# Kernel optimization log

Hardware: AMD Instinct MI355X
Metric: run time of the kernel (lower is better)

The kernel has to match this reference:

```python
import jax, jax.numpy as jnp
import numpy as np

B, P, N, H = 8, 12, 5000, 8
E = 50000
NB = 8
TD0, TD1 = 16, 64
MAX_STEPS = 500


def _proj(x, w1, b1, w2, b2):
    # Projection: Linear -> ReLU -> Linear
    return jax.nn.relu(x @ w1 + b1) @ w2 + b2


def _ln(x, w, b, eps=1e-5):
    # LayerNorm over last two dims [N, H] with affine params [N, H]
    m = jnp.mean(x, axis=(-2, -1), keepdims=True)
    v = jnp.mean((x - m) ** 2, axis=(-2, -1), keepdims=True)
    return (x - m) * jax.lax.rsqrt(v + eps) * w + b


def _time_table():
    # DiffTimeEmbedding buffer: [MAX_STEPS, 2*TD0]
    steps = jnp.arange(MAX_STEPS, dtype=jnp.float32)[:, None]
    dims = jnp.arange(TD0, dtype=jnp.float32)[None, :]
    e = steps * 10.0 ** (dims * 4.0 / TD0)
    return jnp.concatenate([jnp.sin(e), jnp.cos(e)], axis=1)


def setup_inputs() -> dict:
    key = jax.random.key(0)
    ks = jax.random.split(key, 40)
    rn = lambda k, s, sc=0.1: jax.random.normal(k, s, jnp.float32) * sc
    return {
        'x': jax.random.normal(ks[0], (B, P, N), jnp.float32),
        'cond': jax.random.normal(ks[1], (B, P, N, H), jnp.float32),
        'pos': jax.random.normal(ks[2], (N, H), jnp.float32),
        'time': jax.random.randint(ks[3], (B,), 0, MAX_STEPS),
        'edge_index': jax.random.randint(ks[4], (2, E), 0, N),
        'te_w1': rn(ks[5], (2 * TD0, TD1)), 'te_b1': rn(ks[6], (TD1,)),
        'te_w2': rn(ks[7], (TD1, TD1)), 'te_b2': rn(ks[8], (TD1,)),
        'in_w1': rn(ks[9], (1, H)), 'in_b1': rn(ks[10], (H,)),
        'in_w2': rn(ks[11], (H, H)), 'in_b2': rn(ks[12], (H,)),
        'pos_w1': rn(ks[13], (H, H)), 'pos_b1': rn(ks[14], (H,)),
        'pos_w2': rn(ks[15], (H, H)), 'pos_b2': rn(ks[16], (H,)),
        'attn': jax.random.normal(ks[17], (NB + 1, 1), jnp.float32),
        'bt_w1': rn(ks[18], (NB, TD1, H)), 'bt_b1': rn(ks[19], (NB, H)),
        'bt_w2': rn(ks[20], (NB, H, H)), 'bt_b2': rn(ks[21], (NB, H)),
        'bc_w1': rn(ks[22], (NB, H, H)), 'bc_b1': rn(ks[23], (NB, H)),
        'bc_w2': rn(ks[24], (NB, H, H)), 'bc_b2': rn(ks[25], (NB, H)),
        'gn_w': 1.0 + rn(ks[26], (NB, N, H), 0.05), 'gn_b': rn(ks[27], (NB, N, H), 0.05),
        'tn_w': 1.0 + rn(ks[28], (NB, N, H), 0.05), 'tn_b': rn(ks[29], (NB, N, H), 0.05),
        'cv_w': rn(ks[30], (NB, P, P)), 'cv_b': rn(ks[31], (NB, P)),
        'out_w1': rn(ks[32], (H, H)), 'out_b1': rn(ks[33], (H,)),
        'out_w2': rn(ks[34], (H, 1)), 'out_b2': rn(ks[35], (1,)),
    }


def _forward(x, cond, pos, te_w1, te_b1, te_w2, te_b2, in_w1, in_b1, in_w2, in_b2,
             pos_w1, pos_b1, pos_w2, pos_b2, attn, bt_w1, bt_b1, bt_w2, bt_b2,
             bc_w1, bc_b1, bc_w2, bc_b2, gn_w, gn_b, tn_w, tn_b, cv_w, cv_b,
             out_w1, out_b1, out_w2, out_b2, time, edge_index):
    # diffusion-time embedding -> [B, TD1]
    te = _time_table()[time]
    te = jax.nn.silu(te @ te_w1 + te_b1)
    te = jax.nn.silu(te @ te_w2 + te_b2)
    # input + positional projection -> [B, P, N, H]
    h = _proj(x[..., None], in_w1, in_b1, in_w2, in_b2)
    h = h + _proj(pos, pos_w1, pos_b1, pos_w2, pos_b2)
    # LGConv symmetric GCN norm (no self loops), shared across blocks
    src, dst = edge_index[0], edge_index[1]
    deg = jnp.zeros((N,), h.dtype).at[dst].add(1.0)
    dinv = jnp.where(deg > 0, 1.0 / jnp.sqrt(jnp.where(deg > 0, deg, 1.0)), 0.0)
    enorm = dinv[src] * dinv[dst]  # [E]
    skips = [h]
    for i in range(NB):
        t = _proj(te, bt_w1[i], bt_b1[i], bt_w2[i], bt_b2[i])[:, None, None, :]
        c = _proj(cond, bc_w1[i], bc_b1[i], bc_w2[i], bc_b2[i])
        h = _ln(h + c, gn_w[i], gn_b[i])
        # LGConv: gather -> scale -> scatter-add along node dim (-2)
        msg = h[:, :, src, :] * enorm[None, None, :, None]
        h = jnp.zeros_like(h).at[:, :, dst, :].add(msg)
        h = _ln(h + t, tn_w[i], tn_b[i])
        # 1x1 Conv2d over period channels
        h = jnp.einsum('bpnh,qp->bqnh', h, cv_w[i]) + cv_b[i][None, :, None, None]
        skips.append(h)
    s = jnp.stack(skips, axis=-1)  # [B, P, N, H, NB+1]
    a = jax.nn.softmax(attn, axis=0)  # [NB+1, 1]
    h = (s @ a)[..., 0]  # [B, P, N, H]
    return _proj(h, out_w1, out_b1, out_w2, out_b2)[..., 0]  # [B, P, N]


def reference(x, cond, pos, te_w1, te_b1, te_w2, te_b2, in_w1, in_b1, in_w2, in_b2,
              pos_w1, pos_b1, pos_w2, pos_b2, attn, bt_w1, bt_b1, bt_w2, bt_b2,
              bc_w1, bc_b1, bc_w2, bc_b2, gn_w, gn_b, tn_w, tn_b, cv_w, cv_b,
              out_w1, out_b1, out_w2, out_b2, time, edge_index):
    return _forward(x, cond, pos, te_w1, te_b1, te_w2, te_b2, in_w1, in_b1, in_w2, in_b2,
                    pos_w1, pos_b1, pos_w2, pos_b2, attn, bt_w1, bt_b1, bt_w2, bt_b2,
                    bc_w1, bc_b1, bc_w2, bc_b2, gn_w, gn_b, tn_w, tn_b, cv_w, cv_b,
                    out_w1, out_b1, out_w2, out_b2, time, edge_index)
```

## Files before the change

### kernel.cpp

```cpp
#include <hip/hip_runtime.h>
#include <math.h>

#define Bv 8
#define Pv 12
#define Nv 5000
#define Hv 8
#define Ev 50000
#define NBv 8
#define TD1v 64
#define NIMG (Bv * Pv)
#define BLKS_PER_IMG 20

__device__ __constant__ float POW10Q[16] = {
  1.0f, 1.7782794100389228f, 3.1622776601683795f, 5.623413251903491f,
  10.0f, 17.78279410038923f, 31.622776601683793f, 56.23413251903491f,
  100.0f, 177.82794100389228f, 316.22776601683796f, 562.341325190349f,
  1000.0f, 1778.2794100389228f, 3162.2776601683795f, 5623.413251903491f
};

__global__ void k_setup(const int* timei, const float* attn,
                        const float* te_w1, const float* te_b1,
                        const float* te_w2, const float* te_b2,
                        const float* bt_w1, const float* bt_b1,
                        const float* bt_w2, const float* bt_b2,
                        float* t_all, float* a9) {
  __shared__ float te0[Bv][32];
  __shared__ float te1[Bv][64];
  __shared__ float te2[Bv][64];
  int t = threadIdx.x;
  for (int idx = t; idx < Bv * 16; idx += 64) {
    int b = idx >> 4, d = idx & 15;
    float e = (float)timei[b] * POW10Q[d];
    te0[b][d]      = (float)sin((double)e);
    te0[b][d + 16] = (float)cos((double)e);
  }
  __syncthreads();
  for (int idx = t; idx < Bv * 64; idx += 64) {
    int b = idx >> 6, j = idx & 63;
    float s = te_b1[j];
    for (int k = 0; k < 32; ++k) s += te0[b][k] * te_w1[k * 64 + j];
    te1[b][j] = s / (1.0f + expf(-s));
  }
  __syncthreads();
  for (int idx = t; idx < Bv * 64; idx += 64) {
    int b = idx >> 6, j = idx & 63;
    float s = te_b2[j];
    for (int k = 0; k < 64; ++k) s += te1[b][k] * te_w2[k * 64 + j];
    te2[b][j] = s / (1.0f + expf(-s));
  }
  __syncthreads();
  {
    int i = t >> 3, b = t & 7;
    float u[Hv];
    for (int j = 0; j < Hv; ++j) {
      float s = bt_b1[i * Hv + j];
      for (int k = 0; k < TD1v; ++k) s += te2[b][k] * bt_w1[(i * TD1v + k) * Hv + j];
      u[j] = fmaxf(s, 0.0f);
    }
    for (int ch = 0; ch < Hv; ++ch) {
      float s = bt_b2[i * Hv + ch];
      for (int j = 0; j < Hv; ++j) s += u[j] * bt_w2[(i * Hv + j) * Hv + ch];
      t_all[(i * Bv + b) * Hv + ch] = s;
    }
  }
  if (t == 0) {
    float m = attn[0];
    for (int i = 1; i < 9; ++i) m = fmaxf(m, attn[i]);
    float s = 0.f, ex[9];
    for (int i = 0; i < 9; ++i) { ex[i] = expf(attn[i] - m); s += ex[i]; }
    for (int i = 0; i < 9; ++i) a9[i] = ex[i] / s;
  }
}

__global__ void k_posp(const float* pos, const float* pw1, const float* pb1,
                       const float* pw2, const float* pb2, float* posp) {
  int n = blockIdx.x * blockDim.x + threadIdx.x;
  if (n >= Nv) return;
  const float4* pr = (const float4*)(pos + (size_t)n * Hv);
  float4 r0 = pr[0], r1 = pr[1];
  float x[8] = {r0.x, r0.y, r0.z, r0.w, r1.x, r1.y, r1.z, r1.w};
  float u[8];
  #pragma unroll
  for (int j = 0; j < 8; ++j) {
    float s = pb1[j];
    #pragma unroll
    for (int k = 0; k < 8; ++k) s += x[k] * pw1[k * 8 + j];
    u[j] = fmaxf(s, 0.f);
  }
  float o[8];
  #pragma unroll
  for (int ch = 0; ch < 8; ++ch) {
    float s = pb2[ch];
    #pragma unroll
    for (int j = 0; j < 8; ++j) s += u[j] * pw2[j * 8 + ch];
    o[ch] = s;
  }
  float4* po = (float4*)(posp + (size_t)n * Hv);
  po[0] = make_float4(o[0], o[1], o[2], o[3]);
  po[1] = make_float4(o[4], o[5], o[6], o[7]);
}

__global__ void k_zero(float* deg, int* cursor, float* stats) {
  int i = blockIdx.x * blockDim.x + threadIdx.x;
  if (i < Nv) { deg[i] = 0.f; cursor[i] = 0; }
  if (i < NBv * 2 * NIMG * 2) stats[i] = 0.f;
}

__global__ void k_deg(const int* eidx, float* deg) {
  int e = blockIdx.x * blockDim.x + threadIdx.x;
  if (e < Ev) atomicAdd(&deg[eidx[Ev + e]], 1.0f);
}

__global__ void k_dinv(const float* deg, float* dinv) {
  int n = blockIdx.x * blockDim.x + threadIdx.x;
  if (n < Nv) {
    float d = deg[n];
    dinv[n] = d > 0.f ? (float)(1.0 / sqrt((double)d)) : 0.f;
  }
}

__global__ void k_scan(const float* deg, int* row_ptr) {
  __shared__ int buf[1024];
  __shared__ int base_s;
  int t = threadIdx.x;
  if (t == 0) { base_s = 0; row_ptr[0] = 0; }
  __syncthreads();
  for (int c = 0; c < 5; ++c) {
    int i = c * 1024 + t;
    int v = (i < Nv) ? (int)(deg[i] + 0.5f) : 0;
    buf[t] = v;
    __syncthreads();
    for (int off = 1; off < 1024; off <<= 1) {
      int add = (t >= off) ? buf[t - off] : 0;
      __syncthreads();
      buf[t] += add;
      __syncthreads();
    }
    int base = base_s;
    if (i < Nv) row_ptr[i + 1] = base + buf[t];
    __syncthreads();
    if (t == 1023) base_s = base + buf[1023];
    __syncthreads();
  }
}

__global__ void k_csr(const int* eidx, const float* dinv, const int* row_ptr,
                      int* cursor, float2* epack) {
  int e = blockIdx.x * blockDim.x + threadIdx.x;
  if (e >= Ev) return;
  int s = eidx[e], d = eidx[Ev + e];
  int slot = atomicAdd(&cursor[d], 1);
  int pos = row_ptr[d] + slot;
  epack[pos] = make_float2(__int_as_float(s), dinv[s] * dinv[d]);
}

__global__ __launch_bounds__(256) void k_gwb(
    const int* __restrict__ row_ptr, const float2* __restrict__ epack,
    const float* __restrict__ gn_w, const float* __restrict__ gn_b,
    float* __restrict__ Gw, float* __restrict__ Gb) {
  int id = blockIdx.x * 256 + threadIdx.x;
  if (id >= NBv * Nv) return;
  int i = id / Nv, n = id % Nv;
  const float* gw = gn_w + (size_t)i * Nv * Hv;
  const float* gb = gn_b + (size_t)i * Nv * Hv;
  float aw[8] = {0,0,0,0,0,0,0,0}, ab[8] = {0,0,0,0,0,0,0,0};
  int e0 = row_ptr[n], e1 = row_ptr[n + 1];
  for (int e = e0; e < e1; ++e) {
    float2 ep = epack[e];
    int s = __float_as_int(ep.x);
    float w = ep.y;
    const float4* wr = (const float4*)(gw + (size_t)s * Hv);
    const float4* br = (const float4*)(gb + (size_t)s * Hv);
    float4 w0 = wr[0], w1 = wr[1], b0 = br[0], b1 = br[1];
    aw[0] += w * w0.x; aw[1] += w * w0.y; aw[2] += w * w0.z; aw[3] += w * w0.w;
    aw[4] += w * w1.x; aw[5] += w * w1.y; aw[6] += w * w1.z; aw[7] += w * w1.w;
    ab[0] += w * b0.x; ab[1] += w * b0.y; ab[2] += w * b0.z; ab[3] += w * b0.w;
    ab[4] += w * b1.x; ab[5] += w * b1.y; ab[6] += w * b1.z; ab[7] += w * b1.w;
  }
  float4* wo = (float4*)(Gw + (size_t)id * Hv);
  wo[0] = make_float4(aw[0], aw[1], aw[2], aw[3]);
  wo[1] = make_float4(aw[4], aw[5], aw[6], aw[7]);
  float4* bo = (float4*)(Gb + (size_t)id * Hv);
  bo[0] = make_float4(ab[0], ab[1], ab[2], ab[3]);
  bo[1] = make_float4(ab[4], ab[5], ab[6], ab[7]);
}

__global__ void k_init(const float* x, const float* posp,
                       const float* iw1, const float* ib1,
                       const float* iw2, const float* ib2,
                       const float* a9, float* hA, float* acc) {
  int t = blockIdx.x * blockDim.x + threadIdx.x;
  if (t >= Bv * Pv * Nv) return;
  float xv = x[t];
  float u[8];
  #pragma unroll
  for (int j = 0; j < 8; ++j) u[j] = fmaxf(xv * iw1[j] + ib1[j], 0.f);
  int n = t % Nv;
  const float4* pp = (const float4*)(posp + (size_t)n * Hv);
  float4 p0 = pp[0], p1 = pp[1];
  float pv[8] = {p0.x, p0.y, p0.z, p0.w, p1.x, p1.y, p1.z, p1.w};
  float a0 = a9[0];
  float o[8];
  #pragma unroll
  for (int ch = 0; ch < 8; ++ch) {
    float s = ib2[ch];
    #pragma unroll
    for (int j = 0; j < 8; ++j) s += u[j] * iw2[j * 8 + ch];
    o[ch] = s + pv[ch];
  }
  float4* hr = (float4*)(hA + (size_t)t * Hv);
  hr[0] = make_float4(o[0], o[1], o[2], o[3]);
  hr[1] = make_float4(o[4], o[5], o[6], o[7]);
  float4* ar = (float4*)(acc + (size_t)t * Hv);
  ar[0] = make_float4(a0 * o[0], a0 * o[1], a0 * o[2], a0 * o[3]);
  ar[1] = make_float4(a0 * o[4], a0 * o[5], a0 * o[6], a0 * o[7]);
}

__device__ inline void partial_to_stats(float s1, float s2, float* stats_g) {
  #pragma unroll
  for (int off = 32; off > 0; off >>= 1) {
    s1 += __shfl_down(s1, off, 64);
    s2 += __shfl_down(s2, off, 64);
  }
  __shared__ float r1[4], r2[4];
  int wid = threadIdx.x >> 6, lane = threadIdx.x & 63;
  if (lane == 0) { r1[wid] = s1; r2[wid] = s2; }
  __syncthreads();
  if (threadIdx.x == 0) {
    float a = r1[0] + r1[1] + r1[2] + r1[3];
    float b = r2[0] + r2[1] + r2[2] + r2[3];
    atomicAdd(&stats_g[0], a);
    atomicAdd(&stats_g[1], b);
  }
}

__device__ inline void img_swizzle(int bx, int& g, int& chunk) {
  int xcd = bx & 7;
  int local = bx >> 3;
  g = xcd * 12 + local / BLKS_PER_IMG;
  chunk = local % BLKS_PER_IMG;
}

__global__ __launch_bounds__(256) void k_stage1(
    const float* __restrict__ h, const float* __restrict__ cond,
    const float* w1, const float* b1, const float* w2, const float* b2,
    const float* __restrict__ gnw,
    float* __restrict__ vt, float* stats1) {
  __shared__ float lw1[64], lw2[64], lb1[8], lb2[8];
  int t = threadIdx.x;
  if (t < 64) lw1[t] = w1[t];
  else if (t < 128) lw2[t - 64] = w2[t - 64];
  else if (t < 136) lb1[t - 128] = b1[t - 128];
  else if (t < 144) lb2[t - 136] = b2[t - 136];
  __syncthreads();
  int g, chunk;
  img_swizzle(blockIdx.x, g, chunk);
  int n = chunk * 256 + t;
  float s1 = 0.f, s2 = 0.f;
  if (n < Nv) {
    size_t row = ((size_t)g * Nv + n) * Hv;
    const float4* cr = (const float4*)(cond + row);
    float4 c0 = cr[0], c1 = cr[1];
    float xc[8] = {c0.x, c0.y, c0.z, c0.w, c1.x, c1.y, c1.z, c1.w};
    float u[8];
    #pragma unroll
    for (int j = 0; j < 8; ++j) {
      float s = lb1[j];
      #pragma unroll
      for (int k = 0; k < 8; ++k) s += xc[k] * lw1[k * 8 + j];
      u[j] = fmaxf(s, 0.f);
    }
    const float4* hr = (const float4*)(h + row);
    float4 h0 = hr[0], h1 = hr[1];
    float hv[8] = {h0.x, h0.y, h0.z, h0.w, h1.x, h1.y, h1.z, h1.w};
    const float4* gr = (const float4*)(gnw + (size_t)n * Hv);
    float4 g0 = gr[0], g1 = gr[1];
    float gv[8] = {g0.x, g0.y, g0.z, g0.w, g1.x, g1.y, g1.z, g1.w};
    float o[8];
    #pragma unroll
    for (int ch = 0; ch < 8; ++ch) {
      float s = lb2[ch];
      #pragma unroll
      for (int j = 0; j < 8; ++j) s += u[j] * lw2[j * 8 + ch];
      float val = s + hv[ch];
      s1 += val; s2 += val * val;
      o[ch] = val * gv[ch];
    }
    float4* vo = (float4*)(vt + row);
    vo[0] = make_float4(o[0], o[1], o[2], o[3]);
    vo[1] = make_float4(o[4], o[5], o[6], o[7]);
  }
  partial_to_stats(s1, s2, stats1 + (size_t)g * 2);
}

__global__ __launch_bounds__(256) void k_stage2(
    const float* __restrict__ vt, float* __restrict__ v2,
    const int* __restrict__ row_ptr, const float2* __restrict__ epack,
    const float* __restrict__ Gw, const float* __restrict__ Gb,
    const float* __restrict__ stats1, float* stats2,
    const float* __restrict__ tvec) {
  int t = threadIdx.x;
  int g, chunk;
  img_swizzle(blockIdx.x, g, chunk);
  int n = chunk * 256 + t;
  int b = g / Pv;
  float mean = stats1[g * 2] * (1.f / 40000.f);
  float m2   = stats1[g * 2 + 1] * (1.f / 40000.f);
  float var  = m2 - mean * mean;
  float rstd = (float)(1.0 / sqrt((double)var + 1e-5));
  float mrs  = mean * rstd;
  float s1 = 0.f, s2 = 0.f;
  if (n < Nv) {
    size_t ibase = (size_t)g * Nv * Hv;
    float a8[8] = {0.f, 0.f, 0.f, 0.f, 0.f, 0.f, 0.f, 0.f};
    int e0 = row_ptr[n], e1 = row_ptr[n + 1];
    for (int e = e0; e < e1; ++e) {
      float2 ep = epack[e];
      int s = __float_as_int(ep.x);
      float w = ep.y;
      const float4* sr = (const float4*)(vt + ibase + (size_t)s * Hv);
      float4 x0 = sr[0], x1 = sr[1];
      a8[0] += w * x0.x; a8[1] += w * x0.y; a8[2] += w * x0.z; a8[3] += w * x0.w;
      a8[4] += w * x1.x; a8[5] += w * x1.y; a8[6] += w * x1.z; a8[7] += w * x1.w;
    }
    const float4* wr = (const float4*)(Gw + (size_t)n * Hv);
    const float4* br = (const float4*)(Gb + (size_t)n * Hv);
    float4 w0 = wr[0], w1 = wr[1], b0 = br[0], b1 = br[1];
    float gw8[8] = {w0.x, w0.y, w0.z, w0.w, w1.x, w1.y, w1.z, w1.w};
    float gb8[8] = {b0.x, b0.y, b0.z, b0.w, b1.x, b1.y, b1.z, b1.w};
    float o[8];
    #pragma unroll
    for (int ch = 0; ch < 8; ++ch) {
      float val = rstd * a8[ch] - mrs * gw8[ch] + gb8[ch] + tvec[b * Hv + ch];
      o[ch] = val;
      s1 += val; s2 += val * val;
    }
    float4* vo = (float4*)(v2 + ibase + (size_t)n * Hv);
    vo[0] = make_float4(o[0], o[1], o[2], o[3]);
    vo[1] = make_float4(o[4], o[5], o[6], o[7]);
  }
  partial_to_stats(s1, s2, stats2 + (size_t)g * 2);
}

__global__ __launch_bounds__(256) void k_stage3(
    float* __restrict__ v2, float* __restrict__ acc,
    const float* __restrict__ stats2,
    const float* __restrict__ tnw, const float* __restrict__ tnb,
    const float* __restrict__ cw, const float* __restrict__ cb,
    const float* __restrict__ a9, int iblk) {
  __shared__ float scw[144], scb[12], smean[12], srstd[12];
  int t = threadIdx.x;
  int b = blockIdx.x & 7;
  int chunk = blockIdx.x >> 3;
  if (t < 144) scw[t] = cw[t];
  else if (t < 156) scb[t - 144] = cb[t - 144];
  else if (t < 168) {
    int p = t - 156;
    int g = b * Pv + p;
    float mean = stats2[g * 2] * (1.f / 40000.f);
    float m2   = stats2[g * 2 + 1] * (1.f / 40000.f);
    float var  = m2 - mean * mean;
    smean[p] = mean;
    srstd[p] = (float)(1.0 / sqrt((double)var + 1e-5));
  }
  __syncthreads();
  int idx = chunk * 256 + t;
  if (idx >= Nv * 2) return;
  int n = idx >> 1, c4 = idx & 1;
  size_t noff = (size_t)n * Hv + c4 * 4;
  const float4 w4 = *(const float4*)(tnw + noff);
  const float4 b4 = *(const float4*)(tnb + noff);
  size_t strideP = (size_t)Nv * Hv;
  size_t base = (size_t)b * Pv * strideP + noff;
  float4 in[12];
  #pragma unroll
  for (int p = 0; p < 12; ++p) {
    float4 v = *(const float4*)(v2 + base + p * strideP);
    float mean = smean[p], rstd = srstd[p];
    in[p].x = (v.x - mean) * rstd * w4.x + b4.x;
    in[p].y = (v.y - mean) * rstd * w4.y + b4.y;
    in[p].z = (v.z - mean) * rstd * w4.z + b4.z;
    in[p].w = (v.w - mean) * rstd * w4.w + b4.w;
  }
  float ai = a9[iblk + 1];
  #pragma unroll
  for (int q = 0; q < 12; ++q) {
    float4 o = make_float4(scb[q], scb[q], scb[q], scb[q]);
    #pragma unroll
    for (int p = 0; p < 12; ++p) {
      float c = scw[q * 12 + p];
      o.x += c * in[p].x; o.y += c * in[p].y;
      o.z += c * in[p].z; o.w += c * in[p].w;
    }
    size_t off = base + q * strideP;
    *(float4*)(v2 + off) = o;
    float4* ap = (float4*)(acc + off);
    float4 av = *ap;
    av.x += ai * o.x; av.y += ai * o.y; av.z += ai * o.z; av.w += ai * o.w;
    *ap = av;
  }
}

__global__ void k_out(const float* acc, const float* ow1, const float* ob1,
                      const float* ow2, const float* ob2, float* out) {
  int t = blockIdx.x * blockDim.x + threadIdx.x;
  if (t >= Bv * Pv * Nv) return;
  const float4* ar = (const float4*)(acc + (size_t)t * Hv);
  float4 a0 = ar[0], a1 = ar[1];
  float x[8] = {a0.x, a0.y, a0.z, a0.w, a1.x, a1.y, a1.z, a1.w};
  float o = ob2[0];
  #pragma unroll
  for (int j = 0; j < 8; ++j) {
    float s = ob1[j];
    #pragma unroll
    for (int k = 0; k < 8; ++k) s += x[k] * ow1[k * 8 + j];
    o += fmaxf(s, 0.f) * ow2[j];
  }
  out[t] = o;
}

extern "C" void kernel_launch(void* const* d_in, const int* in_sizes, int n_in,
                              void* d_out, int out_size, void* d_ws, size_t ws_size,
                              hipStream_t stream) {
  const float* x      = (const float*)d_in[0];
  const float* cond   = (const float*)d_in[1];
  const float* pos    = (const float*)d_in[2];
  const int*   timei  = (const int*)  d_in[3];
  const int*   eidx   = (const int*)  d_in[4];
  const float* te_w1  = (const float*)d_in[5];
  const float* te_b1  = (const float*)d_in[6];
  const float* te_w2  = (const float*)d_in[7];
  const float* te_b2  = (const float*)d_in[8];
  const float* in_w1  = (const float*)d_in[9];
  const float* in_b1  = (const float*)d_in[10];
  const float* in_w2  = (const float*)d_in[11];
  const float* in_b2  = (const float*)d_in[12];
  const float* pos_w1 = (const float*)d_in[13];
  const float* pos_b1 = (const float*)d_in[14];
  const float* pos_w2 = (const float*)d_in[15];
  const float* pos_b2 = (const float*)d_in[16];
  const float* attn   = (const float*)d_in[17];
  const float* bt_w1  = (const float*)d_in[18];
  const float* bt_b1  = (const float*)d_in[19];
  const float* bt_w2  = (const float*)d_in[20];
  const float* bt_b2  = (const float*)d_in[21];
  const float* bc_w1  = (const float*)d_in[22];
  const float* bc_b1  = (const float*)d_in[23];
  const float* bc_w2  = (const float*)d_in[24];
  const float* bc_b2  = (const float*)d_in[25];
  const float* gn_w   = (const float*)d_in[26];
  const float* gn_b   = (const float*)d_in[27];
  const float* tn_w   = (const float*)d_in[28];
  const float* tn_b   = (const float*)d_in[29];
  const float* cv_w   = (const float*)d_in[30];
  const float* cv_b   = (const float*)d_in[31];
  const float* out_w1 = (const float*)d_in[32];
  const float* out_b1 = (const float*)d_in[33];
  const float* out_w2 = (const float*)d_in[34];
  const float* out_b2 = (const float*)d_in[35];
  float* out = (float*)d_out;

  const size_t HSZ = (size_t)Bv * Pv * Nv * Hv;
  float* ws    = (float*)d_ws;
  float* X     = ws;
  float* Y     = X + HSZ;
  float* acc   = Y + HSZ;
  float* posp  = acc + HSZ;
  float* deg   = posp + Nv * Hv;
  float* dinv  = deg + Nv;
  float* epack = dinv + Nv;
  float* t_all = epack + 2 * Ev;
  float* a9    = t_all + NBv * Bv * Hv;
  float* stats = a9 + 16;
  float* Gw    = stats + NBv * 2 * NIMG * 2;
  float* Gb    = Gw + NBv * Nv * Hv;
  int* row_ptr = (int*)(Gb + NBv * Nv * Hv);
  int* cursor  = row_ptr + Nv + 8;

  k_setup<<<1, 64, 0, stream>>>(timei, attn, te_w1, te_b1, te_w2, te_b2,
                                bt_w1, bt_b1, bt_w2, bt_b2, t_all, a9);
  k_posp<<<(Nv + 255) / 256, 256, 0, stream>>>(pos, pos_w1, pos_b1, pos_w2, pos_b2, posp);
  k_zero<<<(Nv + 255) / 256, 256, 0, stream>>>(deg, cursor, stats);
  k_deg<<<(Ev + 255) / 256, 256, 0, stream>>>(eidx, deg);
  k_dinv<<<(Nv + 255) / 256, 256, 0, stream>>>(deg, dinv);
  k_scan<<<1, 1024, 0, stream>>>(deg, row_ptr);
  k_csr<<<(Ev + 255) / 256, 256, 0, stream>>>(eidx, dinv, row_ptr, cursor, (float2*)epack);
  k_gwb<<<(NBv * Nv + 255) / 256, 256, 0, stream>>>(
      row_ptr, (const float2*)epack, gn_w, gn_b, Gw, Gb);
  k_init<<<(Bv * Pv * Nv + 255) / 256, 256, 0, stream>>>(
      x, posp, in_w1, in_b1, in_w2, in_b2, a9, X, acc);

  for (int i = 0; i < NBv; ++i) {
    float* st1 = stats + (size_t)(i * 2 + 0) * NIMG * 2;
    float* st2 = stats + (size_t)(i * 2 + 1) * NIMG * 2;
    k_stage1<<<NIMG * BLKS_PER_IMG, 256, 0, stream>>>(
        X, cond,
        bc_w1 + i * 64, bc_b1 + i * 8, bc_w2 + i * 64, bc_b2 + i * 8,
        gn_w + (size_t)i * Nv * Hv,
        Y, st1);
    k_stage2<<<NIMG * BLKS_PER_IMG, 256, 0, stream>>>(
        Y, X, row_ptr, (const float2*)epack,
        Gw + (size_t)i * Nv * Hv, Gb + (size_t)i * Nv * Hv,
        st1, st2, t_all + i * Bv * Hv);
    k_stage3<<<8 * 40, 256, 0, stream>>>(
        X, acc, st2,
        tn_w + (size_t)i * Nv * Hv, tn_b + (size_t)i * Nv * Hv,
        cv_w + i * 144, cv_b + i * 12, a9, i);
  }
  k_out<<<(Bv * Pv * Nv + 255) / 256, 256, 0, stream>>>(
      acc, out_w1, out_b1, out_w2, out_b2, out);
}
```

Measured before the change: 657.1 us.

## Switch activations to [B,N,P,H] layout and batch edge gathers across periods

Activation buffers are re-laid out as [B,N,P,H], so one node's 12 periods sit next to each other. Each stage1/stage2 block now handles 10 nodes across all 12 periods, two threads per row. The CSR edge list for a block is staged once in shared memory and reused by all periods, and each neighbour gather reads 384 contiguous bytes instead of scattered rows. Per-period stats are reduced with shared-memory atomics, and nontemporal loads and stores are used for cond, acc and the norm weights; the cost is more global atomics per block and a fallback path when edges exceed the staging buffer.

```diff
diff --git a/kernel.cpp b/kernel.cpp
--- a/kernel.cpp
+++ b/kernel.cpp
@@ -9,7 +9,22 @@
 #define NBv 8
 #define TD1v 64
 #define NIMG (Bv * Pv)
-#define BLKS_PER_IMG 20
+#define NPB 10
+#define TPB 240
+#define EC2 512
+
+#define IDX(b, n, p) ((((size_t)(b) * Nv + (n)) * Pv + (p)) * Hv)
+
+typedef float f4v __attribute__((ext_vector_type(4)));
+
+__device__ inline float4 nt_load4(const float* p) {
+  f4v v = __builtin_nontemporal_load((const f4v*)p);
+  return make_float4(v.x, v.y, v.z, v.w);
+}
+__device__ inline void nt_store4(float* p, float a, float b, float c, float d) {
+  f4v v = {a, b, c, d};
+  __builtin_nontemporal_store(v, (f4v*)p);
+}
 
 __device__ __constant__ float POW10Q[16] = {
   1.0f, 1.7782794100389228f, 3.1622776601683795f, 5.623413251903491f,
@@ -188,14 +203,16 @@
 __global__ void k_init(const float* x, const float* posp,
                        const float* iw1, const float* ib1,
                        const float* iw2, const float* ib2,
-                       const float* a9, float* hA, float* acc) {
+                       const float* a9, float* h, float* acc) {
   int t = blockIdx.x * blockDim.x + threadIdx.x;
   if (t >= Bv * Pv * Nv) return;
-  float xv = x[t];
+  int b = t / (Pv * Nv);
+  int r = t - b * (Pv * Nv);
+  int p = r / Nv, n = r - p * Nv;
+  float xv = __builtin_nontemporal_load(x + t);
   float u[8];
   #pragma unroll
   for (int j = 0; j < 8; ++j) u[j] = fmaxf(xv * iw1[j] + ib1[j], 0.f);
-  int n = t % Nv;
   const float4* pp = (const float4*)(posp + (size_t)n * Hv);
   float4 p0 = pp[0], p1 = pp[1];
   float pv[8] = {p0.x, p0.y, p0.z, p0.w, p1.x, p1.y, p1.z, p1.w};
@@ -208,37 +225,12 @@
     for (int j = 0; j < 8; ++j) s += u[j] * iw2[j * 8 + ch];
     o[ch] = s + pv[ch];
   }
-  float4* hr = (float4*)(hA + (size_t)t * Hv);
+  size_t a = IDX(b, n, p);
+  float4* hr = (float4*)(h + a);
   hr[0] = make_float4(o[0], o[1], o[2], o[3]);
   hr[1] = make_float4(o[4], o[5], o[6], o[7]);
-  float4* ar = (float4*)(acc + (size_t)t * Hv);
-  ar[0] = make_float4(a0 * o[0], a0 * o[1], a0 * o[2], a0 * o[3]);
-  ar[1] = make_float4(a0 * o[4], a0 * o[5], a0 * o[6], a0 * o[7]);
-}
-
-__device__ inline void partial_to_stats(float s1, float s2, float* stats_g) {
-  #pragma unroll
-  for (int off = 32; off > 0; off >>= 1) {
-    s1 += __shfl_down(s1, off, 64);
-    s2 += __shfl_down(s2, off, 64);
-  }
-  __shared__ float r1[4], r2[4];
-  int wid = threadIdx.x >> 6, lane = threadIdx.x & 63;
-  if (lane == 0) { r1[wid] = s1; r2[wid] = s2; }
-  __syncthreads();
-  if (threadIdx.x == 0) {
-    float a = r1[0] + r1[1] + r1[2] + r1[3];
-    float b = r2[0] + r2[1] + r2[2] + r2[3];
-    atomicAdd(&stats_g[0], a);
-    atomicAdd(&stats_g[1], b);
-  }
-}
-
-__device__ inline void img_swizzle(int bx, int& g, int& chunk) {
-  int xcd = bx & 7;
-  int local = bx >> 3;
-  g = xcd * 12 + local / BLKS_PER_IMG;
-  chunk = local % BLKS_PER_IMG;
+  nt_store4(acc + a,     a0 * o[0], a0 * o[1], a0 * o[2], a0 * o[3]);
+  nt_store4(acc + a + 4, a0 * o[4], a0 * o[5], a0 * o[6], a0 * o[7]);
 }
 
 __global__ __launch_bounds__(256) void k_stage1(
@@ -247,50 +239,69 @@
     const float* __restrict__ gnw,
     float* __restrict__ vt, float* stats1) {
   __shared__ float lw1[64], lw2[64], lb1[8], lb2[8];
+  __shared__ float sm1[12], sm2[12];
   int t = threadIdx.x;
+  int b = blockIdx.x & 7;
+  int chunk = blockIdx.x >> 3;
   if (t < 64) lw1[t] = w1[t];
   else if (t < 128) lw2[t - 64] = w2[t - 64];
   else if (t < 136) lb1[t - 128] = b1[t - 128];
   else if (t < 144) lb2[t - 136] = b2[t - 136];
-  __syncthreads();
-  int g, chunk;
-  img_swizzle(blockIdx.x, g, chunk);
-  int n = chunk * 256 + t;
-  float s1 = 0.f, s2 = 0.f;
-  if (n < Nv) {
-    size_t row = ((size_t)g * Nv + n) * Hv;
-    const float4* cr = (const float4*)(cond + row);
-    float4 c0 = cr[0], c1 = cr[1];
-    float xc[8] = {c0.x, c0.y, c0.z, c0.w, c1.x, c1.y, c1.z, c1.w};
+  else if (t < 156) sm1[t - 144] = 0.f;
+  else if (t < 168) sm2[t - 156] = 0.f;
+  __syncthreads();
+  if (t < TPB) {
+    int nl = t / 24, pq = t % 24;
+    int p = pq >> 1, quad = pq & 1;
+    int n = chunk * NPB + nl;
+    size_t caddr = (((size_t)(b * Pv + p)) * Nv + n) * Hv + quad * 4;
+    float4 cme = nt_load4(cond + caddr);
+    float e0 = __shfl_xor(cme.x, 1, 64);
+    float e1 = __shfl_xor(cme.y, 1, 64);
+    float e2 = __shfl_xor(cme.z, 1, 64);
+    float e3 = __shfl_xor(cme.w, 1, 64);
+    float c8[8];
+    if (quad == 0) {
+      c8[0] = cme.x; c8[1] = cme.y; c8[2] = cme.z; c8[3] = cme.w;
+      c8[4] = e0; c8[5] = e1; c8[6] = e2; c8[7] = e3;
+    } else {
+      c8[0] = e0; c8[1] = e1; c8[2] = e2; c8[3] = e3;
+      c8[4] = cme.x; c8[5] = cme.y; c8[6] = cme.z; c8[7] = cme.w;
+    }
     float u[8];
     #pragma unroll
     for (int j = 0; j < 8; ++j) {
       float s = lb1[j];
       #pragma unroll
-      for (int k = 0; k < 8; ++k) s += xc[k] * lw1[k * 8 + j];
+      for (int k = 0; k < 8; ++k) s += c8[k] * lw1[k * 8 + j];
       u[j] = fmaxf(s, 0.f);
     }
-    const float4* hr = (const float4*)(h + row);
-    float4 h0 = hr[0], h1 = hr[1];
-    float hv[8] = {h0.x, h0.y, h0.z, h0.w, h1.x, h1.y, h1.z, h1.w};
-    const float4* gr = (const float4*)(gnw + (size_t)n * Hv);
-    float4 g0 = gr[0], g1 = gr[1];
-    float gv[8] = {g0.x, g0.y, g0.z, g0.w, g1.x, g1.y, g1.z, g1.w};
-    float o[8];
-    #pragma unroll
-    for (int ch = 0; ch < 8; ++ch) {
+    size_t a = IDX(b, n, p) + quad * 4;
+    float4 h4 = *(const float4*)(h + a);
+    float hv[4] = {h4.x, h4.y, h4.z, h4.w};
+    float val[4];
+    float s1 = 0.f, s2 = 0.f;
+    #pragma unroll
+    for (int m = 0; m < 4; ++m) {
+      int ch = quad * 4 + m;
       float s = lb2[ch];
       #pragma unroll
       for (int j = 0; j < 8; ++j) s += u[j] * lw2[j * 8 + ch];
-      float val = s + hv[ch];
-      s1 += val; s2 += val * val;
-      o[ch] = val * gv[ch];
-    }
-    float4* vo = (float4*)(vt + row);
-    vo[0] = make_float4(o[0], o[1], o[2], o[3]);
-    vo[1] = make_float4(o[4], o[5], o[6], o[7]);
-  }
-  partial_to_stats(s1, s2, stats1 + (size_t)g * 2);
+      float v = s + hv[m];
+      val[m] = v;
+      s1 += v; s2 += v * v;
+    }
+    atomicAdd(&sm1[p], s1);
+    atomicAdd(&sm2[p], s2);
+    float4 g4 = *(const float4*)(gnw + (size_t)n * Hv + quad * 4);
+    *(float4*)(vt + a) = make_float4(val[0] * g4.x, val[1] * g4.y,
+                                     val[2] * g4.z, val[3] * g4.w);
+  }
+  __syncthreads();
+  if (t < 12) {
+    atomicAdd(&stats1[(b * Pv + t) * 2],     sm1[t]);
+    atomicAdd(&stats1[(b * Pv + t) * 2 + 1], sm2[t]);
+  }
 }
 
 __global__ __launch_bounds__(256) void k_stage2(
@@ -299,47 +310,70 @@
     const float* __restrict__ Gw, const float* __restrict__ Gb,
     const float* __restrict__ stats1, float* stats2,
     const float* __restrict__ tvec) {
+  __shared__ float2 se[EC2];
+  __shared__ float smean[12], srstd[12], sm1[12], sm2[12];
   int t = threadIdx.x;
-  int g, chunk;
-  img_swizzle(blockIdx.x, g, chunk);
-  int n = chunk * 256 + t;
-  int b = g / Pv;
-  float mean = stats1[g * 2] * (1.f / 40000.f);
-  float m2   = stats1[g * 2 + 1] * (1.f / 40000.f);
-  float var  = m2 - mean * mean;
-  float rstd = (float)(1.0 / sqrt((double)var + 1e-5));
-  float mrs  = mean * rstd;
-  float s1 = 0.f, s2 = 0.f;
-  if (n < Nv) {
-    size_t ibase = (size_t)g * Nv * Hv;
-    float a8[8] = {0.f, 0.f, 0.f, 0.f, 0.f, 0.f, 0.f, 0.f};
+  int b = blockIdx.x & 7;
+  int chunk = blockIdx.x >> 3;
+  int n0 = chunk * NPB;
+  if (t < 12) {
+    int g = b * Pv + t;
+    float m  = stats1[g * 2]     * (1.f / 40000.f);
+    float m2 = stats1[g * 2 + 1] * (1.f / 40000.f);
+    float var = m2 - m * m;
+    smean[t] = m;
+    srstd[t] = (float)(1.0 / sqrt((double)var + 1e-5));
+    sm1[t] = 0.f; sm2[t] = 0.f;
+  }
+  int eb0 = row_ptr[n0];
+  int cnt = row_ptr[n0 + NPB] - eb0;
+  bool staged = (cnt <= EC2);
+  if (staged) {
+    for (int k = t; k < cnt; k += 256) se[k] = epack[eb0 + k];
+  }
+  __syncthreads();
+  if (t < TPB) {
+    int nl = t / 24, pq = t % 24;
+    int p = pq >> 1, quad = pq & 1;
+    int n = n0 + nl;
+    float a0 = 0.f, a1 = 0.f, a2 = 0.f, a3 = 0.f;
     int e0 = row_ptr[n], e1 = row_ptr[n + 1];
-    for (int e = e0; e < e1; ++e) {
-      float2 ep = epack[e];
-      int s = __float_as_int(ep.x);
-      float w = ep.y;
-      const float4* sr = (const float4*)(vt + ibase + (size_t)s * Hv);
-      float4 x0 = sr[0], x1 = sr[1];
-      a8[0] += w * x0.x; a8[1] += w * x0.y; a8[2] += w * x0.z; a8[3] += w * x0.w;
-      a8[4] += w * x1.x; a8[5] += w * x1.y; a8[6] += w * x1.z; a8[7] += w * x1.w;
-    }
-    const float4* wr = (const float4*)(Gw + (size_t)n * Hv);
-    const float4* br = (const float4*)(Gb + (size_t)n * Hv);
-    float4 w0 = wr[0], w1 = wr[1], b0 = br[0], b1 = br[1];
-    float gw8[8] = {w0.x, w0.y, w0.z, w0.w, w1.x, w1.y, w1.z, w1.w};
-    float gb8[8] = {b0.x, b0.y, b0.z, b0.w, b1.x, b1.y, b1.z, b1.w};
-    float o[8];
-    #pragma unroll
-    for (int ch = 0; ch < 8; ++ch) {
-      float val = rstd * a8[ch] - mrs * gw8[ch] + gb8[ch] + tvec[b * Hv + ch];
-      o[ch] = val;
-      s1 += val; s2 += val * val;
-    }
-    float4* vo = (float4*)(v2 + ibase + (size_t)n * Hv);
-    vo[0] = make_float4(o[0], o[1], o[2], o[3]);
-    vo[1] = make_float4(o[4], o[5], o[6], o[7]);
-  }
-  partial_to_stats(s1, s2, stats2 + (size_t)g * 2);
+    size_t bbase = (size_t)b * Nv * Pv * Hv + (size_t)p * Hv + quad * 4;
+    if (staged) {
+      for (int e = e0 - eb0; e < e1 - eb0; ++e) {
+        float2 ep = se[e];
+        int s = __float_as_int(ep.x);
+        float w = ep.y;
+        float4 v = *(const float4*)(vt + bbase + (size_t)s * (Pv * Hv));
+        a0 += w * v.x; a1 += w * v.y; a2 += w * v.z; a3 += w * v.w;
+      }
+    } else {
+      for (int e = e0; e < e1; ++e) {
+        float2 ep = epack[e];
+        int s = __float_as_int(ep.x);
+        float w = ep.y;
+        float4 v = *(const float4*)(vt + bbase + (size_t)s * (Pv * Hv));
+        a0 += w * v.x; a1 += w * v.y; a2 += w * v.z; a3 += w * v.w;
+      }
+    }
+    float mean = smean[p], rstd = srstd[p];
+    float mrs = mean * rstd;
+    float4 gw4 = *(const float4*)(Gw + (size_t)n * Hv + quad * 4);
+    float4 gb4 = *(const float4*)(Gb + (size_t)n * Hv + quad * 4);
+    float4 t4  = *(const float4*)(tvec + b * Hv + quad * 4);
+    float o0 = rstd * a0 - mrs * gw4.x + gb4.x + t4.x;
+    float o1 = rstd * a1 - mrs * gw4.y + gb4.y + t4.y;
+    float o2 = rstd * a2 - mrs * gw4.z + gb4.z + t4.z;
+    float o3 = rstd * a3 - mrs * gw4.w + gb4.w + t4.w;
+    atomicAdd(&sm1[p], o0 + o1 + o2 + o3);
+    atomicAdd(&sm2[p], o0 * o0 + o1 * o1 + o2 * o2 + o3 * o3);
+    *(float4*)(v2 + IDX(b, n, p) + quad * 4) = make_float4(o0, o1, o2, o3);
+  }
+  __syncthreads();
+  if (t < 12) {
+    atomicAdd(&stats2[(b * Pv + t) * 2],     sm1[t]);
+    atomicAdd(&stats2[(b * Pv + t) * 2 + 1], sm2[t]);
+  }
 }
 
 __global__ __launch_bounds__(256) void k_stage3(
@@ -357,7 +391,7 @@
   else if (t < 168) {
     int p = t - 156;
     int g = b * Pv + p;
-    float mean = stats2[g * 2] * (1.f / 40000.f);
+    float mean = stats2[g * 2]     * (1.f / 40000.f);
     float m2   = stats2[g * 2 + 1] * (1.f / 40000.f);
     float var  = m2 - mean * mean;
     smean[p] = mean;
@@ -366,16 +400,14 @@
   __syncthreads();
   int idx = chunk * 256 + t;
   if (idx >= Nv * 2) return;
-  int n = idx >> 1, c4 = idx & 1;
-  size_t noff = (size_t)n * Hv + c4 * 4;
-  const float4 w4 = *(const float4*)(tnw + noff);
-  const float4 b4 = *(const float4*)(tnb + noff);
-  size_t strideP = (size_t)Nv * Hv;
-  size_t base = (size_t)b * Pv * strideP + noff;
+  int n = idx >> 1, quad = idx & 1;
+  const float4 w4 = nt_load4(tnw + (size_t)n * Hv + quad * 4);
+  const float4 b4 = nt_load4(tnb + (size_t)n * Hv + quad * 4);
+  size_t base = IDX(b, n, 0) + quad * 4;
   float4 in[12];
   #pragma unroll
   for (int p = 0; p < 12; ++p) {
-    float4 v = *(const float4*)(v2 + base + p * strideP);
+    float4 v = *(const float4*)(v2 + base + p * Hv);
     float mean = smean[p], rstd = srstd[p];
     in[p].x = (v.x - mean) * rstd * w4.x + b4.x;
     in[p].y = (v.y - mean) * rstd * w4.y + b4.y;
@@ -392,12 +424,11 @@
       o.x += c * in[p].x; o.y += c * in[p].y;
       o.z += c * in[p].z; o.w += c * in[p].w;
     }
-    size_t off = base + q * strideP;
+    size_t off = base + q * Hv;
     *(float4*)(v2 + off) = o;
-    float4* ap = (float4*)(acc + off);
-    float4 av = *ap;
-    av.x += ai * o.x; av.y += ai * o.y; av.z += ai * o.z; av.w += ai * o.w;
-    *ap = av;
+    float4 av = nt_load4(acc + off);
+    nt_store4(acc + off, av.x + ai * o.x, av.y + ai * o.y,
+                         av.z + ai * o.z, av.w + ai * o.w);
   }
 }
 
@@ -405,8 +436,12 @@
                       const float* ow2, const float* ob2, float* out) {
   int t = blockIdx.x * blockDim.x + threadIdx.x;
   if (t >= Bv * Pv * Nv) return;
-  const float4* ar = (const float4*)(acc + (size_t)t * Hv);
-  float4 a0 = ar[0], a1 = ar[1];
+  int b = t / (Pv * Nv);
+  int r = t - b * (Pv * Nv);
+  int p = r / Nv, n = r - p * Nv;
+  size_t a = IDX(b, n, p);
+  float4 a0 = nt_load4(acc + a);
+  float4 a1 = nt_load4(acc + a + 4);
   float x[8] = {a0.x, a0.y, a0.z, a0.w, a1.x, a1.y, a1.z, a1.w};
   float o = ob2[0];
   #pragma unroll
@@ -493,12 +528,12 @@
   for (int i = 0; i < NBv; ++i) {
     float* st1 = stats + (size_t)(i * 2 + 0) * NIMG * 2;
     float* st2 = stats + (size_t)(i * 2 + 1) * NIMG * 2;
-    k_stage1<<<NIMG * BLKS_PER_IMG, 256, 0, stream>>>(
+    k_stage1<<<8 * 500, 256, 0, stream>>>(
         X, cond,
         bc_w1 + i * 64, bc_b1 + i * 8, bc_w2 + i * 64, bc_b2 + i * 8,
         gn_w + (size_t)i * Nv * Hv,
         Y, st1);
-    k_stage2<<<NIMG * BLKS_PER_IMG, 256, 0, stream>>>(
+    k_stage2<<<8 * 500, 256, 0, stream>>>(
         Y, X, row_ptr, (const float2*)epack,
         Gw + (size_t)i * Nv * Hv, Gb + (size_t)i * Nv * Hv,
         st1, st2, t_all + i * Bv * Hv);
```

New measurement: 1.097 ms. 66.9% more time.
